# Optimization experiments

Measured on AMD Instinct MI355X. Metric: run time of the kernel, lower is better.

Reference implementation:

```python
import jax, jax.numpy as jnp
import numpy as np
from jax import lax

B, T, H = 16, 4096, 512

def setup_inputs() -> dict:
    key = jax.random.key(0)
    ks = jax.random.split(key, 10)
    return {
        "query": jax.random.normal(ks[0], (B, 1, H), dtype=jnp.float32),
        "value": jax.random.normal(ks[1], (B, T, H), dtype=jnp.float32),
        "last_attn": jax.random.uniform(ks[2], (B, T), dtype=jnp.float32),
        "conv_w": jax.random.normal(ks[3], (H, 1, 3), dtype=jnp.float32) * 0.05,
        "conv_b": jax.random.normal(ks[4], (H,), dtype=jnp.float32) * 0.05,
        "Wq": jax.random.normal(ks[5], (H, H), dtype=jnp.float32) * (1.0 / np.sqrt(H)),
        "Wv": jax.random.normal(ks[6], (H, H), dtype=jnp.float32) * (1.0 / np.sqrt(H)),
        "bias": jax.random.uniform(ks[7], (H,), minval=-0.1, maxval=0.1, dtype=jnp.float32),
        "w_score": jax.random.normal(ks[8], (1, H), dtype=jnp.float32) * (1.0 / np.sqrt(H)),
        "b_score": jax.random.normal(ks[9], (1,), dtype=jnp.float32) * 0.05,
    }

def reference(query, value, last_attn, conv_w, conv_b, Wq, Wv, bias, w_score, b_score):
    # conv1d over last_attn: (B,1,T) -> (B,H,T), kernel 3, pad 1
    conv = lax.conv_general_dilated(
        last_attn[:, None, :], conv_w, window_strides=(1,), padding="SAME",
        dimension_numbers=("NCH", "OIH", "NCH"))
    conv_attn = conv.transpose(0, 2, 1) + conv_b           # (B,T,H)
    q = jnp.einsum("bqh,oh->bqo", query, Wq)               # (B,1,H), Linear w/o bias: x @ W.T
    v = jnp.einsum("bth,oh->bto", value, Wv)               # (B,T,H)
    e = jnp.tanh(q + v + conv_attn + bias)                 # (B,T,H) broadcast over q_len=1
    score = jnp.einsum("bth,h->bt", e, w_score[0]) + b_score[0]  # (B,T)
    # smoothing=True: sigmoid + L1 normalize
    s = jax.nn.sigmoid(score)
    attn = s / jnp.sum(s, axis=-1, keepdims=True)          # (B,T)
    context = jnp.einsum("bt,bth->bh", attn, value)        # (B,H)
    out = jnp.concatenate([context, query[:, 0, :]], axis=1)  # (B,2H)
    return out, attn
```

## Files before the change

### kernel.cpp

```cpp
#include <hip/hip_runtime.h>
#include <hip/hip_bf16.h>
#include <cstddef>

#define BB 16
#define TT 4096
#define HH 512

typedef _Float16 half8 __attribute__((ext_vector_type(8)));
typedef float f32x4 __attribute__((ext_vector_type(4)));

__device__ __forceinline__ float fast_rcp(float x) { return __builtin_amdgcn_rcpf(x); }

__global__ void prep_kernel(const float* __restrict__ query,
                            const float* __restrict__ conv_b,
                            const float* __restrict__ Wq,
                            const float* __restrict__ Wv,
                            const float* __restrict__ bias,
                            _Float16* __restrict__ Bpack,
                            float* __restrict__ qb,
                            float* __restrict__ ssum,
                            float* __restrict__ ctx) {
    int blk = blockIdx.x;
    int tid = threadIdx.x;
    if (blk < 128) {
        int tn = blk >> 2, kq = blk & 3;
        int kb = kq * 4 + (tid >> 6);
        int lane = tid & 63;
        int n = tn * 16 + (lane & 15);
        int k = kb * 32 + ((lane >> 4) << 3);
        const float4* src = (const float4*)(Wv + (size_t)n * HH + k);
        float4 v0 = src[0], v1 = src[1];
        half8 h = { (_Float16)v0.x, (_Float16)v0.y, (_Float16)v0.z, (_Float16)v0.w,
                    (_Float16)v1.x, (_Float16)v1.y, (_Float16)v1.z, (_Float16)v1.w };
        *(half8*)(Bpack + ((size_t)(kb * 32 + tn) * 64 + lane) * 8) = h;
    } else if (blk < 192) {
        int q = blk - 128;
        int b = q >> 2, oq = q & 3;
        __shared__ float qrow[HH];
        for (int i = tid; i < HH; i += 256) qrow[i] = query[b * HH + i];
        __syncthreads();
        int wave = tid >> 6, lane = tid & 63;
        float4 q1 = *(const float4*)(qrow + lane * 8);
        float4 q2 = *(const float4*)(qrow + lane * 8 + 4);
        for (int i = wave; i < 128; i += 4) {
            int o = oq * 128 + i;
            const float4* w = (const float4*)(Wq + (size_t)o * HH);
            float4 a = w[lane * 2], c = w[lane * 2 + 1];
            float acc = a.x * q1.x + a.y * q1.y + a.z * q1.z + a.w * q1.w
                      + c.x * q2.x + c.y * q2.y + c.z * q2.z + c.w * q2.w;
            #pragma unroll
            for (int off = 1; off < 64; off <<= 1) acc += __shfl_xor(acc, off, 64);
            if (lane == 0) qb[b * HH + o] = acc + bias[o] + conv_b[o];
        }
    } else {
        for (int i = tid; i < BB; i += 256) ssum[i] = 0.f;
        for (int i = tid; i < BB * HH; i += 256) ctx[i] = 0.f;
    }
}

__global__ __launch_bounds__(512, 4) void gemm_fused_kernel(
        const float* __restrict__ value,
        const float* __restrict__ last_attn,
        const float* __restrict__ conv_w,
        const float* __restrict__ w_score,
        const float* __restrict__ b_score,
        const _Float16* __restrict__ Bpack,
        const float* __restrict__ qb,
        float* __restrict__ sbuf,
        float* __restrict__ ssum,
        float* __restrict__ ctx) {
    extern __shared__ _Float16 As[];
    __shared__ float sred[64][9];
    __shared__ float s_lds[64];
    __shared__ float la_s[66];

    int tid = threadIdx.x;
    int blk = blockIdx.x;
    int b = blk >> 6;
    int t0 = (blk & 63) << 6;

    int lane = tid & 63, ng = tid >> 6;
    int quad = lane >> 4, lm = lane & 15;

    const _Float16* bp = Bpack + (size_t)(ng * 2) * 512 + lane * 8;
    half8 breg[4][2];
    #pragma unroll
    for (int kb = 0; kb < 2; ++kb)
        #pragma unroll
        for (int nt = 0; nt < 2; ++nt)
            breg[kb][nt] = *(const half8*)(bp + kb * 16384 + nt * 512);
    bp += 2 * 16384;

    float qvv[2], c0v[2], c1v[2], c2v[2], wvv[2];
    #pragma unroll
    for (int nt = 0; nt < 2; ++nt) {
        int o = ng * 32 + nt * 16 + lm;
        qvv[nt] = qb[b * HH + o];
        c0v[nt] = conv_w[o * 3 + 0];
        c1v[nt] = conv_w[o * 3 + 1];
        c2v[nt] = conv_w[o * 3 + 2];
        wvv[nt] = w_score[o];
    }

    if (tid < 66) {
        int tg = t0 - 1 + tid;
        la_s[tid] = (tg >= 0 && tg < TT) ? last_attn[b * TT + tg] : 0.f;
    }

    {
        int row = tid >> 3, cc = tid & 7;
        const float4* pA = (const float4*)(value + ((size_t)(b * TT + t0 + row)) * HH);
        #pragma unroll
        for (int u = 0; u < 8; ++u) {
            int c_log = cc + u * 8;
            float4 v0 = pA[2 * c_log], v1 = pA[2 * c_log + 1];
            int cph = c_log ^ (row & 7);
            half8 h = { (_Float16)v0.x, (_Float16)v0.y, (_Float16)v0.z, (_Float16)v0.w,
                        (_Float16)v1.x, (_Float16)v1.y, (_Float16)v1.z, (_Float16)v1.w };
            *(half8*)(As + row * 512 + cph * 8) = h;
        }
    }

    f32x4 acc[4][2];
    #pragma unroll
    for (int mt = 0; mt < 4; ++mt)
        #pragma unroll
        for (int nt = 0; nt < 2; ++nt) { f32x4 z = {0.f,0.f,0.f,0.f}; acc[mt][nt] = z; }

    __syncthreads();

    #pragma unroll 4
    for (int kb = 0; kb < 16; ++kb) {
        if (kb < 14) {
            #pragma unroll
            for (int nt = 0; nt < 2; ++nt)
                breg[(kb + 2) & 3][nt] = *(const half8*)(bp + nt * 512);
            bp += 16384;
        }
        #pragma unroll
        for (int mt = 0; mt < 4; ++mt) {
            int tr = mt * 16 + lm;
            int cph = ((kb << 2) + quad) ^ (tr & 7);
            half8 a = *(const half8*)(As + tr * 512 + cph * 8);
            #pragma unroll
            for (int nt = 0; nt < 2; ++nt)
                acc[mt][nt] = __builtin_amdgcn_mfma_f32_16x16x32_f16(a, breg[kb & 3][nt], acc[mt][nt], 0, 0, 0);
        }
    }

    #pragma unroll
    for (int mt = 0; mt < 4; ++mt) {
        float rsj[4];
        #pragma unroll
        for (int j = 0; j < 4; ++j) {
            int tl = mt * 16 + quad * 4 + j;
            float lam = la_s[tl];
            float la0 = la_s[tl + 1];
            float lap = la_s[tl + 2];
            float r = 0.f;
            #pragma unroll
            for (int nt = 0; nt < 2; ++nt) {
                float act = acc[mt][nt][j] + qvv[nt]
                          + c0v[nt] * lam + c1v[nt] * la0 + c2v[nt] * lap;
                act = fminf(15.f, fmaxf(-15.f, act));
                float e2 = __expf(2.f * act);
                r += (1.f - 2.f * fast_rcp(e2 + 1.f)) * wvv[nt];
            }
            #pragma unroll
            for (int off = 1; off < 16; off <<= 1) r += __shfl_xor(r, off, 64);
            rsj[j] = r;
        }
        if (lm == 0)
            #pragma unroll
            for (int j = 0; j < 4; ++j)
                sred[mt * 16 + quad * 4 + j][ng] = rsj[j];
    }
    __syncthreads();

    if (tid < 64) {
        float sc = b_score[0];
        #pragma unroll
        for (int k = 0; k < 8; ++k) sc += sred[tid][k];
        float s = fast_rcp(1.f + __expf(-sc));
        s_lds[tid] = s;
        sbuf[b * TT + t0 + tid] = s;
        float tot = s;
        #pragma unroll
        for (int off = 1; off < 64; off <<= 1) tot += __shfl_xor(tot, off, 64);
        if (tid == 0) atomicAdd(&ssum[b], tot);
    }
    __syncthreads();

    {
        int h = tid;
        int cl = h >> 3, j = h & 7;
        float a = 0.f;
        #pragma unroll 8
        for (int t2 = 0; t2 < 64; ++t2) {
            int cph = cl ^ (t2 & 7);
            a += s_lds[t2] * (float)As[t2 * 512 + cph * 8 + j];
        }
        atomicAdd(&ctx[b * HH + h], a);
    }
}

__global__ void finalize_kernel(const float* __restrict__ query,
                                const float* __restrict__ ctx,
                                const float* __restrict__ sbuf,
                                const float* __restrict__ ssum,
                                float* __restrict__ out) {
    int idx = blockIdx.x * 256 + threadIdx.x;
    if (idx < BB * 2 * HH) {
        int b = idx >> 10, c = idx & 1023;
        float v;
        if (c < HH) v = ctx[b * HH + c] / ssum[b];
        else        v = query[b * HH + (c - HH)];
        out[idx] = v;
    } else {
        int j = idx - BB * 2 * HH;
        int b = j >> 12, t = j & 4095;
        out[idx] = sbuf[b * TT + t] / ssum[b];
    }
}

extern "C" void kernel_launch(void* const* d_in, const int* in_sizes, int n_in,
                              void* d_out, int out_size, void* d_ws, size_t ws_size,
                              hipStream_t stream) {
    const float* query     = (const float*)d_in[0];
    const float* value     = (const float*)d_in[1];
    const float* last_attn = (const float*)d_in[2];
    const float* conv_w    = (const float*)d_in[3];
    const float* conv_b    = (const float*)d_in[4];
    const float* Wq        = (const float*)d_in[5];
    const float* Wv        = (const float*)d_in[6];
    const float* bias      = (const float*)d_in[7];
    const float* w_score   = (const float*)d_in[8];
    const float* b_score   = (const float*)d_in[9];

    char* ws = (char*)d_ws;
    _Float16* Bpack = (_Float16*)ws;
    float* qb     = (float*)(ws + 524288);
    float* sbuf   = (float*)(ws + 557056);
    float* ssum   = (float*)(ws + 819200);
    float* ctx    = (float*)(ws + 819264);
    float* out    = (float*)d_out;

    static bool attr_set = false;
    if (!attr_set) {
        hipFuncSetAttribute((const void*)gemm_fused_kernel,
                            hipFuncAttributeMaxDynamicSharedMemorySize, 65536);
        attr_set = true;
    }

    prep_kernel<<<193, 256, 0, stream>>>(query, conv_b, Wq, Wv, bias, Bpack, qb, ssum, ctx);
    gemm_fused_kernel<<<1024, 512, 65536, stream>>>(value, last_attn, conv_w, w_score,
                                                    b_score, Bpack, qb, sbuf, ssum, ctx);
    finalize_kernel<<<320, 256, 0, stream>>>(query, ctx, sbuf, ssum, out);
}
```

Measured before the change: 252.7 us.

## Split A-tile load into halves to overlap second half loads with first-half MFMAs

The fp32 value tile is now loaded into registers in two halves. The first half is converted and stored to LDS before the first eight k-steps of MFMA run, and the second half is stored afterwards behind an extra barrier, so global load latency for the second half overlaps compute. The B-operand register prefetch drops from two steps ahead to one, which lowers register pressure. In exchange the kernel holds 16 extra float4 registers live across the first MFMA phase and adds a barrier.

```diff
diff --git a/kernel.cpp b/kernel.cpp
--- a/kernel.cpp
+++ b/kernel.cpp
@@ -83,13 +83,99 @@
     int quad = lane >> 4, lm = lane & 15;
 
     const _Float16* bp = Bpack + (size_t)(ng * 2) * 512 + lane * 8;
-    half8 breg[4][2];
-    #pragma unroll
-    for (int kb = 0; kb < 2; ++kb)
+    half8 breg[2][2];
+    #pragma unroll
+    for (int nt = 0; nt < 2; ++nt)
+        breg[0][nt] = *(const half8*)(bp + nt * 512);
+    bp += 16384;
+
+    if (tid < 66) {
+        int tg = t0 - 1 + tid;
+        la_s[tid] = (tg >= 0 && tg < TT) ? last_attn[b * TT + tg] : 0.f;
+    }
+
+    int row = tid >> 3, cc = tid & 7;
+    const float4* pA = (const float4*)(value + ((size_t)(b * TT + t0 + row)) * HH);
+
+    float4 p1[8];
+    #pragma unroll
+    for (int u = 0; u < 4; ++u) {
+        int c_log = cc + u * 8;
+        p1[2 * u]     = pA[2 * c_log];
+        p1[2 * u + 1] = pA[2 * c_log + 1];
+    }
+    float4 p2[8];
+    #pragma unroll
+    for (int u = 0; u < 4; ++u) {
+        int c_log = cc + (u + 4) * 8;
+        p2[2 * u]     = pA[2 * c_log];
+        p2[2 * u + 1] = pA[2 * c_log + 1];
+    }
+    #pragma unroll
+    for (int u = 0; u < 4; ++u) {
+        int c_log = cc + u * 8;
+        int cph = c_log ^ (row & 7);
+        float4 v0 = p1[2 * u], v1 = p1[2 * u + 1];
+        half8 h = { (_Float16)v0.x, (_Float16)v0.y, (_Float16)v0.z, (_Float16)v0.w,
+                    (_Float16)v1.x, (_Float16)v1.y, (_Float16)v1.z, (_Float16)v1.w };
+        *(half8*)(As + row * 512 + cph * 8) = h;
+    }
+
+    f32x4 acc[4][2];
+    #pragma unroll
+    for (int mt = 0; mt < 4; ++mt)
+        #pragma unroll
+        for (int nt = 0; nt < 2; ++nt) { f32x4 z = {0.f,0.f,0.f,0.f}; acc[mt][nt] = z; }
+
+    __syncthreads();
+
+    #pragma unroll 2
+    for (int kb = 0; kb < 8; ++kb) {
         #pragma unroll
         for (int nt = 0; nt < 2; ++nt)
-            breg[kb][nt] = *(const half8*)(bp + kb * 16384 + nt * 512);
-    bp += 2 * 16384;
+            breg[(kb + 1) & 1][nt] = *(const half8*)(bp + nt * 512);
+        bp += 16384;
+        #pragma unroll
+        for (int mt = 0; mt < 4; ++mt) {
+            int tr = mt * 16 + lm;
+            int cph = ((kb << 2) + quad) ^ (tr & 7);
+            half8 a = *(const half8*)(As + tr * 512 + cph * 8);
+            #pragma unroll
+            for (int nt = 0; nt < 2; ++nt)
+                acc[mt][nt] = __builtin_amdgcn_mfma_f32_16x16x32_f16(a, breg[kb & 1][nt], acc[mt][nt], 0, 0, 0);
+        }
+    }
+
+    #pragma unroll
+    for (int u = 0; u < 4; ++u) {
+        int c_log = cc + (u + 4) * 8;
+        int cph = c_log ^ (row & 7);
+        float4 v0 = p2[2 * u], v1 = p2[2 * u + 1];
+        half8 h = { (_Float16)v0.x, (_Float16)v0.y, (_Float16)v0.z, (_Float16)v0.w,
+                    (_Float16)v1.x, (_Float16)v1.y, (_Float16)v1.z, (_Float16)v1.w };
+        *(half8*)(As + row * 512 + cph * 8) = h;
+    }
+
+    __syncthreads();
+
+    #pragma unroll 2
+    for (int kb = 8; kb < 16; ++kb) {
+        if (kb < 15) {
+            #pragma unroll
+            for (int nt = 0; nt < 2; ++nt)
+                breg[(kb + 1) & 1][nt] = *(const half8*)(bp + nt * 512);
+            bp += 16384;
+        }
+        #pragma unroll
+        for (int mt = 0; mt < 4; ++mt) {
+            int tr = mt * 16 + lm;
+            int cph = ((kb << 2) + quad) ^ (tr & 7);
+            half8 a = *(const half8*)(As + tr * 512 + cph * 8);
+            #pragma unroll
+            for (int nt = 0; nt < 2; ++nt)
+                acc[mt][nt] = __builtin_amdgcn_mfma_f32_16x16x32_f16(a, breg[kb & 1][nt], acc[mt][nt], 0, 0, 0);
+        }
+    }
 
     float qvv[2], c0v[2], c1v[2], c2v[2], wvv[2];
     #pragma unroll
@@ -101,53 +187,6 @@
         c2v[nt] = conv_w[o * 3 + 2];
         wvv[nt] = w_score[o];
     }
-
-    if (tid < 66) {
-        int tg = t0 - 1 + tid;
-        la_s[tid] = (tg >= 0 && tg < TT) ? last_attn[b * TT + tg] : 0.f;
-    }
-
-    {
-        int row = tid >> 3, cc = tid & 7;
-        const float4* pA = (const float4*)(value + ((size_t)(b * TT + t0 + row)) * HH);
-        #pragma unroll
-        for (int u = 0; u < 8; ++u) {
-            int c_log = cc + u * 8;
-            float4 v0 = pA[2 * c_log], v1 = pA[2 * c_log + 1];
-            int cph = c_log ^ (row & 7);
-            half8 h = { (_Float16)v0.x, (_Float16)v0.y, (_Float16)v0.z, (_Float16)v0.w,
-                        (_Float16)v1.x, (_Float16)v1.y, (_Float16)v1.z, (_Float16)v1.w };
-            *(half8*)(As + row * 512 + cph * 8) = h;
-        }
-    }
-
-    f32x4 acc[4][2];
-    #pragma unroll
-    for (int mt = 0; mt < 4; ++mt)
-        #pragma unroll
-        for (int nt = 0; nt < 2; ++nt) { f32x4 z = {0.f,0.f,0.f,0.f}; acc[mt][nt] = z; }
-
-    __syncthreads();
-
-    #pragma unroll 4
-    for (int kb = 0; kb < 16; ++kb) {
-        if (kb < 14) {
-            #pragma unroll
-            for (int nt = 0; nt < 2; ++nt)
-                breg[(kb + 2) & 3][nt] = *(const half8*)(bp + nt * 512);
-            bp += 16384;
-        }
-        #pragma unroll
-        for (int mt = 0; mt < 4; ++mt) {
-            int tr = mt * 16 + lm;
-            int cph = ((kb << 2) + quad) ^ (tr & 7);
-            half8 a = *(const half8*)(As + tr * 512 + cph * 8);
-            #pragma unroll
-            for (int nt = 0; nt < 2; ++nt)
-                acc[mt][nt] = __builtin_amdgcn_mfma_f32_16x16x32_f16(a, breg[kb & 3][nt], acc[mt][nt], 0, 0, 0);
-        }
-    }
-
     #pragma unroll
     for (int mt = 0; mt < 4; ++mt) {
         float rsj[4];
@@ -234,8 +273,9 @@
     const float* Wq        = (const float*)d_in[5];
     const float* Wv        = (const float*)d_in[6];
     const float* bias      = (const float*)d_in[7];
+    const float* b_score_  = (const float*)d_in[9];
     const float* w_score   = (const float*)d_in[8];
-    const float* b_score   = (const float*)d_in[9];
+    const float* b_score   = b_score_;
 
     char* ws = (char*)d_ws;
     _Float16* Bpack = (_Float16*)ws;
```

Result: no change. 256.9 us (+1.7%).

## Persistent tiles with double-buffered async global-to-LDS loads and register-resident Wv

Applied to the files above, without the earlier changes.

The fused GEMM kernel now runs 256 blocks, and each block walks 8 tiles of 32 timesteps. Tiles of fp32 `value` are staged into two LDS buffers with global_load_lds, and explicit vmcnt waits and barriers let the next tile load while the current one computes. The packed Wv fragments are held entirely in registers, loaded once per block, and the fp32 LDS data is converted to fp16 at MFMA operand read time. Per-block partial context and score sums are accumulated in registers before a single set of atomics. The cost is about 129 KB of LDS per block, so only one block fits per CU, plus higher register pressure and hand-written waitcnt logic that depends on in-order memory counters.

```diff
diff --git a/kernel.cpp b/kernel.cpp
--- a/kernel.cpp
+++ b/kernel.cpp
@@ -10,6 +10,10 @@
 typedef float f32x4 __attribute__((ext_vector_type(4)));
 
 __device__ __forceinline__ float fast_rcp(float x) { return __builtin_amdgcn_rcpf(x); }
+
+#define ASM_VMCNT8() { asm volatile("s_waitcnt vmcnt(8)" ::: "memory"); __builtin_amdgcn_sched_barrier(0); }
+#define ASM_VMCNT0() { asm volatile("s_waitcnt vmcnt(0)" ::: "memory"); __builtin_amdgcn_sched_barrier(0); }
+#define ASM_LGKM0()  { asm volatile("s_waitcnt lgkmcnt(0)" ::: "memory"); __builtin_amdgcn_sched_barrier(0); }
 
 __global__ void prep_kernel(const float* __restrict__ query,
                             const float* __restrict__ conv_b,
@@ -58,7 +62,7 @@
     }
 }
 
-__global__ __launch_bounds__(512, 4) void gemm_fused_kernel(
+__global__ __launch_bounds__(512, 2) void gemm_fused_kernel(
         const float* __restrict__ value,
         const float* __restrict__ last_attn,
         const float* __restrict__ conv_w,
@@ -69,27 +73,25 @@
         float* __restrict__ sbuf,
         float* __restrict__ ssum,
         float* __restrict__ ctx) {
-    extern __shared__ _Float16 As[];
-    __shared__ float sred[64][9];
-    __shared__ float s_lds[64];
-    __shared__ float la_s[66];
+    extern __shared__ float Asf[];
+    __shared__ float sred[32][9];
+    __shared__ float s_lds[32];
 
     int tid = threadIdx.x;
     int blk = blockIdx.x;
-    int b = blk >> 6;
-    int t0 = (blk & 63) << 6;
+    int b = blk >> 4;
+    int ts = blk & 15;
 
     int lane = tid & 63, ng = tid >> 6;
     int quad = lane >> 4, lm = lane & 15;
 
-    const _Float16* bp = Bpack + (size_t)(ng * 2) * 512 + lane * 8;
-    half8 breg[4][2];
+    const _Float16* bp0 = Bpack + (size_t)(ng * 2) * 512 + lane * 8;
+    half8 breg[16][2];
     #pragma unroll
-    for (int kb = 0; kb < 2; ++kb)
+    for (int kb = 0; kb < 16; ++kb)
         #pragma unroll
         for (int nt = 0; nt < 2; ++nt)
-            breg[kb][nt] = *(const half8*)(bp + kb * 16384 + nt * 512);
-    bp += 2 * 16384;
+            breg[kb][nt] = *(const half8*)(bp0 + (size_t)kb * 16384 + nt * 512);
 
     float qvv[2], c0v[2], c1v[2], c2v[2], wvv[2];
     #pragma unroll
@@ -101,106 +103,131 @@
         c2v[nt] = conv_w[o * 3 + 2];
         wvv[nt] = w_score[o];
     }
-
-    if (tid < 66) {
-        int tg = t0 - 1 + tid;
-        la_s[tid] = (tg >= 0 && tg < TT) ? last_attn[b * TT + tg] : 0.f;
-    }
-
-    {
-        int row = tid >> 3, cc = tid & 7;
-        const float4* pA = (const float4*)(value + ((size_t)(b * TT + t0 + row)) * HH);
-        #pragma unroll
-        for (int u = 0; u < 8; ++u) {
-            int c_log = cc + u * 8;
-            float4 v0 = pA[2 * c_log], v1 = pA[2 * c_log + 1];
-            int cph = c_log ^ (row & 7);
-            half8 h = { (_Float16)v0.x, (_Float16)v0.y, (_Float16)v0.z, (_Float16)v0.w,
-                        (_Float16)v1.x, (_Float16)v1.y, (_Float16)v1.z, (_Float16)v1.w };
-            *(half8*)(As + row * 512 + cph * 8) = h;
-        }
-    }
-
-    f32x4 acc[4][2];
-    #pragma unroll
-    for (int mt = 0; mt < 4; ++mt)
-        #pragma unroll
-        for (int nt = 0; nt < 2; ++nt) { f32x4 z = {0.f,0.f,0.f,0.f}; acc[mt][nt] = z; }
-
-    __syncthreads();
-
-    #pragma unroll 4
-    for (int kb = 0; kb < 16; ++kb) {
-        if (kb < 14) {
-            #pragma unroll
-            for (int nt = 0; nt < 2; ++nt)
-                breg[(kb + 2) & 3][nt] = *(const half8*)(bp + nt * 512);
-            bp += 16384;
-        }
-        #pragma unroll
-        for (int mt = 0; mt < 4; ++mt) {
-            int tr = mt * 16 + lm;
-            int cph = ((kb << 2) + quad) ^ (tr & 7);
-            half8 a = *(const half8*)(As + tr * 512 + cph * 8);
-            #pragma unroll
-            for (int nt = 0; nt < 2; ++nt)
-                acc[mt][nt] = __builtin_amdgcn_mfma_f32_16x16x32_f16(a, breg[kb & 3][nt], acc[mt][nt], 0, 0, 0);
-        }
-    }
-
-    #pragma unroll
-    for (int mt = 0; mt < 4; ++mt) {
-        float rsj[4];
-        #pragma unroll
-        for (int j = 0; j < 4; ++j) {
-            int tl = mt * 16 + quad * 4 + j;
-            float lam = la_s[tl];
-            float la0 = la_s[tl + 1];
-            float lap = la_s[tl + 2];
-            float r = 0.f;
-            #pragma unroll
-            for (int nt = 0; nt < 2; ++nt) {
-                float act = acc[mt][nt][j] + qvv[nt]
-                          + c0v[nt] * lam + c1v[nt] * la0 + c2v[nt] * lap;
-                act = fminf(15.f, fmaxf(-15.f, act));
-                float e2 = __expf(2.f * act);
-                r += (1.f - 2.f * fast_rcp(e2 + 1.f)) * wvv[nt];
-            }
-            #pragma unroll
-            for (int off = 1; off < 16; off <<= 1) r += __shfl_xor(r, off, 64);
-            rsj[j] = r;
-        }
-        if (lm == 0)
-            #pragma unroll
-            for (int j = 0; j < 4; ++j)
-                sred[mt * 16 + quad * 4 + j][ng] = rsj[j];
-    }
-    __syncthreads();
-
+    float bsc = b_score[0];
+
+    auto STAGE = [&](int buf, int tj) {
+        const float* gbase = value + ((size_t)b * TT + (size_t)tj * 32) * HH;
+        float* lbase = Asf + buf * 16512;
+        #pragma unroll
+        for (int rr = 0; rr < 4; ++rr) {
+            int row = ng * 4 + rr;
+            #pragma unroll
+            for (int hf = 0; hf < 2; ++hf) {
+                const float* g = gbase + (size_t)row * HH + hf * 256 + lane * 4;
+                float* l = lbase + row * 516 + hf * 256;
+                __builtin_amdgcn_global_load_lds(
+                    (const __attribute__((address_space(1))) void*)g,
+                    (__attribute__((address_space(3))) void*)l, 16, 0, 0);
+            }
+        }
+    };
+
+    STAGE(0, ts);
+    STAGE(1, ts + 16);
+
+    float ctx_acc = 0.f;
+    float tot_acc = 0.f;
+
+    for (int j = 0; j < 8; ++j) {
+        int tj = ts + 16 * j;
+        int t0 = tj * 32;
+        float* As = Asf + (j & 1) * 16512;
+
+        if (j < 7) { ASM_VMCNT8(); } else { ASM_VMCNT0(); }
+        __builtin_amdgcn_s_barrier();
+
+        float la[2][6];
+        #pragma unroll
+        for (int mt = 0; mt < 2; ++mt) {
+            int tg0 = t0 + mt * 16 + quad * 4;
+            #pragma unroll
+            for (int u = 0; u < 6; ++u) {
+                int tg = tg0 - 1 + u;
+                la[mt][u] = (tg >= 0 && tg < TT) ? last_attn[(size_t)b * TT + tg] : 0.f;
+            }
+        }
+
+        f32x4 acc[2][2];
+        #pragma unroll
+        for (int mt = 0; mt < 2; ++mt)
+            #pragma unroll
+            for (int nt = 0; nt < 2; ++nt) { f32x4 z = {0.f,0.f,0.f,0.f}; acc[mt][nt] = z; }
+
+        #pragma unroll
+        for (int kb = 0; kb < 16; ++kb) {
+            #pragma unroll
+            for (int mt = 0; mt < 2; ++mt) {
+                const float* p = As + (mt * 16 + lm) * 516 + kb * 32 + quad * 8;
+                f32x4 a0 = *(const f32x4*)p;
+                f32x4 a1 = *(const f32x4*)(p + 4);
+                half8 a = { (_Float16)a0.x, (_Float16)a0.y, (_Float16)a0.z, (_Float16)a0.w,
+                            (_Float16)a1.x, (_Float16)a1.y, (_Float16)a1.z, (_Float16)a1.w };
+                #pragma unroll
+                for (int nt = 0; nt < 2; ++nt)
+                    acc[mt][nt] = __builtin_amdgcn_mfma_f32_16x16x32_f16(a, breg[kb][nt], acc[mt][nt], 0, 0, 0);
+            }
+        }
+
+        #pragma unroll
+        for (int mt = 0; mt < 2; ++mt) {
+            float rsj[4];
+            #pragma unroll
+            for (int jj = 0; jj < 4; ++jj) {
+                float lam = la[mt][jj];
+                float la0 = la[mt][jj + 1];
+                float lap = la[mt][jj + 2];
+                float r = 0.f;
+                #pragma unroll
+                for (int nt = 0; nt < 2; ++nt) {
+                    float act = acc[mt][nt][jj] + qvv[nt]
+                              + c0v[nt] * lam + c1v[nt] * la0 + c2v[nt] * lap;
+                    act = fminf(15.f, fmaxf(-15.f, act));
+                    float e2 = __expf(2.f * act);
+                    r += (1.f - 2.f * fast_rcp(e2 + 1.f)) * wvv[nt];
+                }
+                #pragma unroll
+                for (int off = 1; off < 16; off <<= 1) r += __shfl_xor(r, off, 64);
+                rsj[jj] = r;
+            }
+            if (lm == 0)
+                #pragma unroll
+                for (int jj = 0; jj < 4; ++jj)
+                    sred[mt * 16 + quad * 4 + jj][ng] = rsj[jj];
+        }
+        ASM_LGKM0();
+        __builtin_amdgcn_s_barrier();
+
+        if (tid < 32) {
+            float sc = bsc;
+            #pragma unroll
+            for (int k = 0; k < 8; ++k) sc += sred[tid][k];
+            float s = fast_rcp(1.f + __expf(-sc));
+            s_lds[tid] = s;
+            sbuf[(size_t)b * TT + t0 + tid] = s;
+            tot_acc += s;
+        }
+        ASM_LGKM0();
+        __builtin_amdgcn_s_barrier();
+
+        {
+            float a = 0.f;
+            #pragma unroll 8
+            for (int t2 = 0; t2 < 32; ++t2)
+                a += s_lds[t2] * As[t2 * 516 + tid];
+            ctx_acc += a;
+        }
+        ASM_LGKM0();
+        __builtin_amdgcn_s_barrier();
+
+        if (j < 6) STAGE(j & 1, ts + 16 * (j + 2));
+    }
+
+    atomicAdd(&ctx[b * HH + tid], ctx_acc);
     if (tid < 64) {
-        float sc = b_score[0];
-        #pragma unroll
-        for (int k = 0; k < 8; ++k) sc += sred[tid][k];
-        float s = fast_rcp(1.f + __expf(-sc));
-        s_lds[tid] = s;
-        sbuf[b * TT + t0 + tid] = s;
-        float tot = s;
+        float tot = tot_acc;
         #pragma unroll
         for (int off = 1; off < 64; off <<= 1) tot += __shfl_xor(tot, off, 64);
         if (tid == 0) atomicAdd(&ssum[b], tot);
-    }
-    __syncthreads();
-
-    {
-        int h = tid;
-        int cl = h >> 3, j = h & 7;
-        float a = 0.f;
-        #pragma unroll 8
-        for (int t2 = 0; t2 < 64; ++t2) {
-            int cph = cl ^ (t2 & 7);
-            a += s_lds[t2] * (float)As[t2 * 512 + cph * 8 + j];
-        }
-        atomicAdd(&ctx[b * HH + h], a);
     }
 }
 
@@ -248,12 +275,12 @@
     static bool attr_set = false;
     if (!attr_set) {
         hipFuncSetAttribute((const void*)gemm_fused_kernel,
-                            hipFuncAttributeMaxDynamicSharedMemorySize, 65536);
+                            hipFuncAttributeMaxDynamicSharedMemorySize, 132096);
         attr_set = true;
     }
 
     prep_kernel<<<193, 256, 0, stream>>>(query, conv_b, Wq, Wv, bias, Bpack, qb, ssum, ctx);
-    gemm_fused_kernel<<<1024, 512, 65536, stream>>>(value, last_attn, conv_w, w_score,
+    gemm_fused_kernel<<<256, 512, 132096, stream>>>(value, last_attn, conv_w, w_score,
                                                     b_score, Bpack, qb, sbuf, ssum, ctx);
     finalize_kernel<<<320, 256, 0, stream>>>(query, ctx, sbuf, ssum, out);
 }
```

New measurement: 257.9 us. 2.1% more time.

## Make fused GEMM kernel persistent with double-buffered LDS and register-resident weights

Applied to the files above, without the earlier changes.

Each block now handles four 64-row tiles instead of one, with 256 blocks in place of 1024. The full Wv fragment slice stays in registers for the whole block, and the next value tile is loaded from global memory and converted into a second LDS buffer while MFMA and epilogue work run on the current one. Context and score-sum partials accumulate in registers and are written with one atomic per block, and the score broadcast uses shuffles instead of LDS. The cost is 128KB of LDS and higher register pressure with launch bounds lowered to 2. That leaves fewer resident blocks and only 256 blocks for the device, which may limit latency hiding.

```diff
diff --git a/kernel.cpp b/kernel.cpp
--- a/kernel.cpp
+++ b/kernel.cpp
@@ -10,6 +10,9 @@
 typedef float f32x4 __attribute__((ext_vector_type(4)));
 
 __device__ __forceinline__ float fast_rcp(float x) { return __builtin_amdgcn_rcpf(x); }
+
+#define ASM_LGKM0() { asm volatile("s_waitcnt lgkmcnt(0)" ::: "memory"); __builtin_amdgcn_sched_barrier(0); }
+#define PIN8(a,b,c,d,e,f,g,h) asm volatile("" : "+v"(a), "+v"(b), "+v"(c), "+v"(d), "+v"(e), "+v"(f), "+v"(g), "+v"(h))
 
 __global__ void prep_kernel(const float* __restrict__ query,
                             const float* __restrict__ conv_b,
@@ -58,7 +61,7 @@
     }
 }
 
-__global__ __launch_bounds__(512, 4) void gemm_fused_kernel(
+__global__ __launch_bounds__(512, 2) void gemm_fused_kernel(
         const float* __restrict__ value,
         const float* __restrict__ last_attn,
         const float* __restrict__ conv_w,
@@ -71,25 +74,24 @@
         float* __restrict__ ctx) {
     extern __shared__ _Float16 As[];
     __shared__ float sred[64][9];
-    __shared__ float s_lds[64];
     __shared__ float la_s[66];
 
     int tid = threadIdx.x;
     int blk = blockIdx.x;
-    int b = blk >> 6;
-    int t0 = (blk & 63) << 6;
+    int b = blk >> 4;
+    int ts = blk & 15;
 
     int lane = tid & 63, ng = tid >> 6;
     int quad = lane >> 4, lm = lane & 15;
-
-    const _Float16* bp = Bpack + (size_t)(ng * 2) * 512 + lane * 8;
-    half8 breg[4][2];
+    int srow = tid >> 3, scc = tid & 7;
+
+    const _Float16* bp0 = Bpack + (size_t)(ng * 2) * 512 + lane * 8;
+    half8 breg[16][2];
     #pragma unroll
-    for (int kb = 0; kb < 2; ++kb)
-        #pragma unroll
-        for (int nt = 0; nt < 2; ++nt)
-            breg[kb][nt] = *(const half8*)(bp + kb * 16384 + nt * 512);
-    bp += 2 * 16384;
+    for (int kb = 0; kb < 16; ++kb) {
+        breg[kb][0] = *(const half8*)(bp0 + (size_t)kb * 16384);
+        breg[kb][1] = *(const half8*)(bp0 + (size_t)kb * 16384 + 512);
+    }
 
     float qvv[2], c0v[2], c1v[2], c2v[2], wvv[2];
     #pragma unroll
@@ -101,106 +103,174 @@
         c2v[nt] = conv_w[o * 3 + 2];
         wvv[nt] = w_score[o];
     }
-
-    if (tid < 66) {
-        int tg = t0 - 1 + tid;
-        la_s[tid] = (tg >= 0 && tg < TT) ? last_attn[b * TT + tg] : 0.f;
-    }
+    float bsc = b_score[0];
 
     {
-        int row = tid >> 3, cc = tid & 7;
-        const float4* pA = (const float4*)(value + ((size_t)(b * TT + t0 + row)) * HH);
+        const float4* pA = (const float4*)(value + ((size_t)b * TT + (size_t)ts * 64 + srow) * HH);
+        float4 g[16];
         #pragma unroll
         for (int u = 0; u < 8; ++u) {
-            int c_log = cc + u * 8;
-            float4 v0 = pA[2 * c_log], v1 = pA[2 * c_log + 1];
-            int cph = c_log ^ (row & 7);
+            int c = scc + u * 8;
+            g[2 * u] = pA[2 * c]; g[2 * u + 1] = pA[2 * c + 1];
+        }
+        #pragma unroll
+        for (int u = 0; u < 8; ++u) {
+            int c = scc + u * 8;
+            int cph = c ^ (srow & 7);
+            float4 v0 = g[2 * u], v1 = g[2 * u + 1];
             half8 h = { (_Float16)v0.x, (_Float16)v0.y, (_Float16)v0.z, (_Float16)v0.w,
                         (_Float16)v1.x, (_Float16)v1.y, (_Float16)v1.z, (_Float16)v1.w };
-            *(half8*)(As + row * 512 + cph * 8) = h;
-        }
-    }
-
-    f32x4 acc[4][2];
-    #pragma unroll
-    for (int mt = 0; mt < 4; ++mt)
-        #pragma unroll
-        for (int nt = 0; nt < 2; ++nt) { f32x4 z = {0.f,0.f,0.f,0.f}; acc[mt][nt] = z; }
-
-    __syncthreads();
-
-    #pragma unroll 4
-    for (int kb = 0; kb < 16; ++kb) {
-        if (kb < 14) {
-            #pragma unroll
-            for (int nt = 0; nt < 2; ++nt)
-                breg[(kb + 2) & 3][nt] = *(const half8*)(bp + nt * 512);
-            bp += 16384;
-        }
+            *(half8*)(As + srow * 512 + cph * 8) = h;
+        }
+        if (tid < 66) {
+            int tg = ts * 64 - 1 + tid;
+            la_s[tid] = (tg >= 0 && tg < TT) ? last_attn[(size_t)b * TT + tg] : 0.f;
+        }
+    }
+
+    float ctx_acc = 0.f, tot_acc = 0.f;
+
+    for (int j = 0; j < 4; ++j) {
+        int cur = j & 1;
+        int t0 = (ts + 16 * j) * 64;
+        _Float16* Ab = As + cur * 32768;
+        _Float16* An = As + (cur ^ 1) * 32768;
+
+        ASM_LGKM0();
+        __builtin_amdgcn_s_barrier();
+
+        PIN8(breg[0][0],breg[0][1],breg[1][0],breg[1][1],breg[2][0],breg[2][1],breg[3][0],breg[3][1]);
+        PIN8(breg[4][0],breg[4][1],breg[5][0],breg[5][1],breg[6][0],breg[6][1],breg[7][0],breg[7][1]);
+        PIN8(breg[8][0],breg[8][1],breg[9][0],breg[9][1],breg[10][0],breg[10][1],breg[11][0],breg[11][1]);
+        PIN8(breg[12][0],breg[12][1],breg[13][0],breg[13][1],breg[14][0],breg[14][1],breg[15][0],breg[15][1]);
+
+        const float4* pAn = (const float4*)(value + ((size_t)b * TT + (size_t)(ts + 16 * (j + 1)) * 64 + srow) * HH);
+        float4 g0[8];
+        if (j < 3) {
+            #pragma unroll
+            for (int u = 0; u < 4; ++u) {
+                int c = scc + u * 8;
+                g0[2 * u] = pAn[2 * c]; g0[2 * u + 1] = pAn[2 * c + 1];
+            }
+            __builtin_amdgcn_sched_barrier(0);
+        }
+
+        f32x4 acc[4][2];
         #pragma unroll
         for (int mt = 0; mt < 4; ++mt) {
-            int tr = mt * 16 + lm;
-            int cph = ((kb << 2) + quad) ^ (tr & 7);
-            half8 a = *(const half8*)(As + tr * 512 + cph * 8);
-            #pragma unroll
-            for (int nt = 0; nt < 2; ++nt)
-                acc[mt][nt] = __builtin_amdgcn_mfma_f32_16x16x32_f16(a, breg[kb & 3][nt], acc[mt][nt], 0, 0, 0);
-        }
-    }
-
-    #pragma unroll
-    for (int mt = 0; mt < 4; ++mt) {
-        float rsj[4];
-        #pragma unroll
-        for (int j = 0; j < 4; ++j) {
-            int tl = mt * 16 + quad * 4 + j;
-            float lam = la_s[tl];
-            float la0 = la_s[tl + 1];
-            float lap = la_s[tl + 2];
-            float r = 0.f;
-            #pragma unroll
-            for (int nt = 0; nt < 2; ++nt) {
-                float act = acc[mt][nt][j] + qvv[nt]
-                          + c0v[nt] * lam + c1v[nt] * la0 + c2v[nt] * lap;
-                act = fminf(15.f, fmaxf(-15.f, act));
-                float e2 = __expf(2.f * act);
-                r += (1.f - 2.f * fast_rcp(e2 + 1.f)) * wvv[nt];
-            }
-            #pragma unroll
-            for (int off = 1; off < 16; off <<= 1) r += __shfl_xor(r, off, 64);
-            rsj[j] = r;
-        }
-        if (lm == 0)
-            #pragma unroll
-            for (int j = 0; j < 4; ++j)
-                sred[mt * 16 + quad * 4 + j][ng] = rsj[j];
-    }
-    __syncthreads();
-
+            f32x4 z = {0.f, 0.f, 0.f, 0.f};
+            acc[mt][0] = z; acc[mt][1] = z;
+        }
+        #pragma unroll
+        for (int kb = 0; kb < 16; ++kb) {
+            #pragma unroll
+            for (int mt = 0; mt < 4; ++mt) {
+                int tr = mt * 16 + lm;
+                int cph = ((kb << 2) + quad) ^ (tr & 7);
+                half8 a = *(const half8*)(Ab + tr * 512 + cph * 8);
+                acc[mt][0] = __builtin_amdgcn_mfma_f32_16x16x32_f16(a, breg[kb][0], acc[mt][0], 0, 0, 0);
+                acc[mt][1] = __builtin_amdgcn_mfma_f32_16x16x32_f16(a, breg[kb][1], acc[mt][1], 0, 0, 0);
+            }
+        }
+        __builtin_amdgcn_sched_barrier(0);
+
+        if (j < 3) {
+            #pragma unroll
+            for (int u = 0; u < 4; ++u) {
+                int c = scc + u * 8;
+                int cph = c ^ (srow & 7);
+                float4 v0 = g0[2 * u], v1 = g0[2 * u + 1];
+                half8 h = { (_Float16)v0.x, (_Float16)v0.y, (_Float16)v0.z, (_Float16)v0.w,
+                            (_Float16)v1.x, (_Float16)v1.y, (_Float16)v1.z, (_Float16)v1.w };
+                *(half8*)(An + srow * 512 + cph * 8) = h;
+            }
+        }
+
+        #pragma unroll
+        for (int mt = 0; mt < 4; ++mt) {
+            float rsj[4];
+            #pragma unroll
+            for (int jx = 0; jx < 4; ++jx) {
+                int tl = mt * 16 + quad * 4 + jx;
+                float lam = la_s[tl];
+                float la0 = la_s[tl + 1];
+                float lap = la_s[tl + 2];
+                float r = 0.f;
+                #pragma unroll
+                for (int nt = 0; nt < 2; ++nt) {
+                    float act = acc[mt][nt][jx] + qvv[nt]
+                              + c0v[nt] * lam + c1v[nt] * la0 + c2v[nt] * lap;
+                    act = fminf(15.f, fmaxf(-15.f, act));
+                    float e2 = __expf(2.f * act);
+                    r += (1.f - 2.f * fast_rcp(e2 + 1.f)) * wvv[nt];
+                }
+                #pragma unroll
+                for (int off = 1; off < 16; off <<= 1) r += __shfl_xor(r, off, 64);
+                rsj[jx] = r;
+            }
+            if (lm == 0)
+                #pragma unroll
+                for (int jx = 0; jx < 4; ++jx)
+                    sred[mt * 16 + quad * 4 + jx][ng] = rsj[jx];
+        }
+        ASM_LGKM0();
+        __builtin_amdgcn_s_barrier();
+
+        float4 g1[8];
+        if (j < 3) {
+            #pragma unroll
+            for (int u = 0; u < 4; ++u) {
+                int c = scc + (u + 4) * 8;
+                g1[2 * u] = pAn[2 * c]; g1[2 * u + 1] = pAn[2 * c + 1];
+            }
+            if (tid < 66) {
+                int tg = (ts + 16 * (j + 1)) * 64 - 1 + tid;
+                la_s[tid] = (tg >= 0 && tg < TT) ? last_attn[(size_t)b * TT + tg] : 0.f;
+            }
+            __builtin_amdgcn_sched_barrier(0);
+        }
+
+        float sc = bsc;
+        #pragma unroll
+        for (int k = 0; k < 8; ++k) sc += sred[lane][k];
+        float s = fast_rcp(1.f + __expf(-sc));
+        if (tid < 64) {
+            sbuf[(size_t)b * TT + t0 + tid] = s;
+            tot_acc += s;
+        }
+
+        {
+            int cl = tid >> 3, jj = tid & 7;
+            float a = 0.f;
+            #pragma unroll 8
+            for (int t2 = 0; t2 < 64; ++t2) {
+                float sv = __shfl(s, t2, 64);
+                int cph = cl ^ (t2 & 7);
+                a += sv * (float)Ab[t2 * 512 + cph * 8 + jj];
+            }
+            ctx_acc += a;
+        }
+        __builtin_amdgcn_sched_barrier(0);
+
+        if (j < 3) {
+            #pragma unroll
+            for (int u = 0; u < 4; ++u) {
+                int c = scc + (u + 4) * 8;
+                int cph = c ^ (srow & 7);
+                float4 v0 = g1[2 * u], v1 = g1[2 * u + 1];
+                half8 h = { (_Float16)v0.x, (_Float16)v0.y, (_Float16)v0.z, (_Float16)v0.w,
+                            (_Float16)v1.x, (_Float16)v1.y, (_Float16)v1.z, (_Float16)v1.w };
+                *(half8*)(An + srow * 512 + cph * 8) = h;
+            }
+        }
+    }
+
+    atomicAdd(&ctx[b * HH + tid], ctx_acc);
     if (tid < 64) {
-        float sc = b_score[0];
-        #pragma unroll
-        for (int k = 0; k < 8; ++k) sc += sred[tid][k];
-        float s = fast_rcp(1.f + __expf(-sc));
-        s_lds[tid] = s;
-        sbuf[b * TT + t0 + tid] = s;
-        float tot = s;
+        float tot = tot_acc;
         #pragma unroll
         for (int off = 1; off < 64; off <<= 1) tot += __shfl_xor(tot, off, 64);
         if (tid == 0) atomicAdd(&ssum[b], tot);
-    }
-    __syncthreads();
-
-    {
-        int h = tid;
-        int cl = h >> 3, j = h & 7;
-        float a = 0.f;
-        #pragma unroll 8
-        for (int t2 = 0; t2 < 64; ++t2) {
-            int cph = cl ^ (t2 & 7);
-            a += s_lds[t2] * (float)As[t2 * 512 + cph * 8 + j];
-        }
-        atomicAdd(&ctx[b * HH + h], a);
     }
 }
 
@@ -248,12 +318,12 @@
     static bool attr_set = false;
     if (!attr_set) {
         hipFuncSetAttribute((const void*)gemm_fused_kernel,
-                            hipFuncAttributeMaxDynamicSharedMemorySize, 65536);
+                            hipFuncAttributeMaxDynamicSharedMemorySize, 131072);
         attr_set = true;
     }
 
     prep_kernel<<<193, 256, 0, stream>>>(query, conv_b, Wq, Wv, bias, Bpack, qb, ssum, ctx);
-    gemm_fused_kernel<<<1024, 512, 65536, stream>>>(value, last_attn, conv_w, w_score,
+    gemm_fused_kernel<<<256, 512, 131072, stream>>>(value, last_attn, conv_w, w_score,
                                                     b_score, Bpack, qb, sbuf, ssum, ctx);
     finalize_kernel<<<320, 256, 0, stream>>>(query, ctx, sbuf, ssum, out);
 }
```

New measurement: 326.2 us. 29.1% more time.
